# Kernel optimization log

Hardware: AMD Instinct MI355X
Metric: run time of the kernel (lower is better)

The kernel has to match this reference:

```python
import jax, jax.numpy as jnp
import numpy as np

IN_FEATURES = 256
OUT_FEATURES = 128
ALPHA = 0.2  # LeakyReLU negative slope
NEG_INF = -9e15
N_NODES = 8192


def _xavier_uniform(key, shape, gain):
    fan_in, fan_out = shape[0], shape[1]
    limit = gain * np.sqrt(6.0 / (fan_in + fan_out))
    return jax.random.uniform(key, shape, jnp.float32, -limit, limit)


def setup_inputs() -> dict:
    key = jax.random.key(0)
    k_h, k_adj, k_W, k_a = jax.random.split(key, 4)
    h = jax.random.normal(k_h, (N_NODES, IN_FEATURES), dtype=jnp.float32)
    adj = jax.random.randint(k_adj, (N_NODES, N_NODES), 0, 2, dtype=jnp.int32)
    W = _xavier_uniform(k_W, (IN_FEATURES, OUT_FEATURES), gain=1.414)
    a = _xavier_uniform(k_a, (2 * OUT_FEATURES, 1), gain=1.414)
    return {"h": h, "adj": adj, "W": W, "a": a}


def reference(h, adj, W, a):
    # Wh: (N, F_out)
    Wh = h @ W
    # Decompose a = [a1; a2]; e_ij = leakyrelu(Wh_i . a1 + Wh_j . a2)
    # == the original concat([Wh_i, Wh_j]) @ a, without the O(N^2*2F) tensor.
    a1 = a[:OUT_FEATURES, 0]  # (F_out,)
    a2 = a[OUT_FEATURES:, 0]  # (F_out,)
    src = Wh @ a1  # (N,)
    dst = Wh @ a2  # (N,)
    e = jax.nn.leaky_relu(src[:, None] + dst[None, :], negative_slope=ALPHA)  # (N, N)
    attention = jnp.where(adj > 0, e, NEG_INF)
    attention = jax.nn.softmax(attention, axis=1)
    # dropout p=0.0 (eval) -> identity
    h_prime = attention @ Wh  # (N, F_out)
    return jax.nn.elu(h_prime)  # concat=True
```

## Files before the change

kernel.cpp:

```cpp
#include <hip/hip_runtime.h>
#include <hip/hip_bf16.h>

#define N_NODES 8192
#define IN_F    256
#define OUT_F   128
#define ALPHA_S 0.2f

typedef __attribute__((ext_vector_type(8))) short  short8;
typedef __attribute__((ext_vector_type(4))) float  floatx4;
typedef __attribute__((ext_vector_type(4))) int    intx4;
typedef __attribute__((ext_vector_type(4))) float  fx4;

static __device__ __forceinline__ float bf2f(short s) {
    union { unsigned int i; float f; } u;
    u.i = ((unsigned int)(unsigned short)s) << 16;
    return u.f;
}
static __device__ __forceinline__ short f2bf(float f) {
    union { float f; unsigned int i; } u; u.f = f;
    unsigned int r = u.i + 0x7FFFu + ((u.i >> 16) & 1u);
    return (short)(r >> 16);
}

__global__ void k_detect(const unsigned int* __restrict__ hw, int* __restrict__ flag) {
    const int lane = threadIdx.x;
    unsigned int w = hw[lane * 31];
    int e = (w >> 7) & 0xFF;
    unsigned long long b = __ballot(e >= 100 && e <= 140);
    if (lane == 0) *flag = (__popcll(b) >= 40) ? 1 : 0;
}

static __device__ __forceinline__ void load8(const short* p, float* o) {
    short8 v = *(const short8*)p;
#pragma unroll
    for (int j = 0; j < 8; ++j) o[j] = bf2f(v[j]);
}
static __device__ __forceinline__ void load8(const float* p, float* o) {
    float4 v0 = *(const float4*)p;
    float4 v1 = *(const float4*)(p + 4);
    o[0] = v0.x; o[1] = v0.y; o[2] = v0.z; o[3] = v0.w;
    o[4] = v1.x; o[5] = v1.y; o[6] = v1.z; o[7] = v1.w;
}
static __device__ __forceinline__ float to_f(short s)  { return bf2f(s); }
static __device__ __forceinline__ float to_f(float f)  { return f; }

template<typename T>
static __device__ void wh_impl(const T* __restrict__ h, const T* __restrict__ W,
                               const T* __restrict__ a,
                               short* __restrict__ WhT, float* __restrict__ src,
                               float* __restrict__ dst,
                               float* h_tile, short* wh_t, int t, int r_base)
{
    {
        const T* g = h + (size_t)r_base * IN_F;
        float tmp[8];
        load8(g + t * 16, tmp);
#pragma unroll
        for (int j = 0; j < 8; ++j) h_tile[t * 16 + j] = tmp[j];
        load8(g + t * 16 + 8, tmp);
#pragma unroll
        for (int j = 0; j < 8; ++j) h_tile[t * 16 + 8 + j] = tmp[j];
    }
    __syncthreads();

    const int r0   = t >> 4;
    const int fgrp = t & 15;
    const int f0   = fgrp * 8;

    float acc[8];
#pragma unroll
    for (int j = 0; j < 8; ++j) acc[j] = 0.f;

#pragma unroll 4
    for (int k = 0; k < IN_F; ++k) {
        float hf = h_tile[r0 * IN_F + k];
        float wv[8];
        load8(W + (size_t)k * OUT_F + f0, wv);
#pragma unroll
        for (int j = 0; j < 8; ++j)
            acc[j] = fmaf(hf, wv[j], acc[j]);
    }

    float sp = 0.f, dp = 0.f;
#pragma unroll
    for (int j = 0; j < 8; ++j) {
        sp = fmaf(acc[j], to_f(a[f0 + j]), sp);
        dp = fmaf(acc[j], to_f(a[OUT_F + f0 + j]), dp);
    }
#pragma unroll
    for (int m = 1; m < 16; m <<= 1) {
        sp += __shfl_xor(sp, m, 64);
        dp += __shfl_xor(dp, m, 64);
    }
    if (fgrp == 0) {
        src[r_base + r0] = sp;
        dst[r_base + r0] = dp;
    }

#pragma unroll
    for (int j = 0; j < 8; ++j)
        wh_t[(f0 + j) * 32 + r0] = f2bf(acc[j]);
    __syncthreads();
    {
        const int f    = t >> 2;
        const int half = t & 3;
        *(short8*)(WhT + (size_t)f * N_NODES + r_base + half * 8) =
            *(const short8*)&wh_t[f * 32 + half * 8];
    }
}

__global__ __launch_bounds__(512) void k_wh(
    const void* __restrict__ h, const void* __restrict__ W, const void* __restrict__ a,
    const int* __restrict__ flag,
    short* __restrict__ WhT, float* __restrict__ src, float* __restrict__ dst)
{
    __shared__ float h_tile[32 * IN_F];
    __shared__ short wh_t[OUT_F * 32];
    const int t = threadIdx.x;
    const int r_base = blockIdx.x * 32;
    if (*flag)
        wh_impl<short>((const short*)h, (const short*)W, (const short*)a,
                       WhT, src, dst, h_tile, wh_t, t, r_base);
    else
        wh_impl<float>((const float*)h, (const float*)W, (const float*)a,
                       WhT, src, dst, h_tile, wh_t, t, r_base);
}

#define BM 32
#define BK 128
#define WPAD (BK + 8)
#define NIT (N_NODES / BK)

__global__ __launch_bounds__(512) void k_attn(
    const int*   __restrict__ adj,
    const short* __restrict__ WhT,
    const float* __restrict__ src,
    const float* __restrict__ dstv,
    float* __restrict__ out)
{
    __shared__ short wbuf[2][BM * WPAD];
    __shared__ float denom_s[BM];

    const int t    = threadIdx.x;
    const int lane = t & 63;
    const int wave = t >> 6;
    const int r0   = blockIdx.x * BM;

    const int sm  = t >> 4;
    const int sk0 = (t & 15) * 8;
    const float srow = src[r0 + sm];
    const size_t adj_base = (size_t)(r0 + sm) * N_NODES;

    const int ln15 = lane & 15;
    const int q    = lane >> 4;
    const int f0   = wave * 16;
    const short* bbase = WhT + (size_t)(f0 + ln15) * N_NODES + q * 8;

    floatx4 acc0 = {0.f, 0.f, 0.f, 0.f};
    floatx4 acc1 = {0.f, 0.f, 0.f, 0.f};
    floatx4 dac0 = {0.f, 0.f, 0.f, 0.f};
    floatx4 dac1 = {0.f, 0.f, 0.f, 0.f};
    short8 ones;
#pragma unroll
    for (int j = 0; j < 8; ++j) ones[j] = (short)0x3F80;

    auto stage = [&](int it, int buf) {
        const size_t j0 = (size_t)it * BK;
        intx4 m0 = *(const intx4*)(adj + adj_base + j0 + sk0);
        intx4 m1 = *(const intx4*)(adj + adj_base + j0 + sk0 + 4);
        fx4  d0  = *(const fx4*)(dstv + j0 + sk0);
        fx4  d1  = *(const fx4*)(dstv + j0 + sk0 + 4);
        short8 wv;
#pragma unroll
        for (int e = 0; e < 4; ++e) {
            float x = srow + d0[e];
            float l = fmaxf(x, ALPHA_S * x);
            wv[e] = (m0[e] > 0) ? f2bf(__expf(l)) : (short)0;
        }
#pragma unroll
        for (int e = 0; e < 4; ++e) {
            float x = srow + d1[e];
            float l = fmaxf(x, ALPHA_S * x);
            wv[4 + e] = (m1[e] > 0) ? f2bf(__expf(l)) : (short)0;
        }
        *(short8*)&wbuf[buf][sm * WPAD + sk0] = wv;
    };

    auto compute = [&](int it, int buf) {
        const int j0 = it * BK;
        const short* ab = &wbuf[buf][ln15 * WPAD + q * 8];
        const short* bb = bbase + j0;
#pragma unroll
        for (int ks = 0; ks < 4; ++ks) {
            short8 afr0 = *(const short8*)(ab + ks * 32);
            short8 afr1 = *(const short8*)(ab + 16 * WPAD + ks * 32);
            short8 bfr  = *(const short8*)(bb + ks * 32);
            acc0 = __builtin_amdgcn_mfma_f32_16x16x32_bf16(afr0, bfr, acc0, 0, 0, 0);
            acc1 = __builtin_amdgcn_mfma_f32_16x16x32_bf16(afr1, bfr, acc1, 0, 0, 0);
            if (wave == 0) {
                dac0 = __builtin_amdgcn_mfma_f32_16x16x32_bf16(afr0, ones, dac0, 0, 0, 0);
                dac1 = __builtin_amdgcn_mfma_f32_16x16x32_bf16(afr1, ones, dac1, 0, 0, 0);
            }
        }
    };

    stage(0, 0);
    for (int it = 0; it < NIT; ++it) {
        const int p = it & 1;
        __syncthreads();
        if (it + 1 < NIT) stage(it + 1, p ^ 1);
        compute(it, p);
    }

    if (wave == 0 && ln15 == 0) {
#pragma unroll
        for (int r = 0; r < 4; ++r) {
            denom_s[q * 4 + r]      = dac0[r];
            denom_s[16 + q * 4 + r] = dac1[r];
        }
    }
    __syncthreads();
#pragma unroll
    for (int r = 0; r < 4; ++r) {
        const int row0 = q * 4 + r;
        float v0 = acc0[r] / denom_s[row0];
        v0 = v0 > 0.f ? v0 : (__expf(v0) - 1.f);
        out[(size_t)(r0 + row0) * OUT_F + f0 + ln15] = v0;

        const int row1 = 16 + q * 4 + r;
        float v1 = acc1[r] / denom_s[row1];
        v1 = v1 > 0.f ? v1 : (__expf(v1) - 1.f);
        out[(size_t)(r0 + row1) * OUT_F + f0 + ln15] = v1;
    }
}

extern "C" void kernel_launch(void* const* d_in, const int* in_sizes, int n_in,
                              void* d_out, int out_size, void* d_ws, size_t ws_size,
                              hipStream_t stream) {
    const void* h   = d_in[0];
    const int*  adj = (const int*)d_in[1];
    const void* W   = d_in[2];
    const void* a   = d_in[3];
    float* out = (float*)d_out;

    char* ws    = (char*)d_ws;
    int*   flag = (int*)ws;
    short* WhT  = (short*)(ws + 256);
    float* src  = (float*)(ws + 256 + (size_t)OUT_F * N_NODES * 2);
    float* dst  = src + N_NODES;

    k_detect<<<1, 64, 0, stream>>>((const unsigned int*)h, flag);
    k_wh<<<256, 512, 0, stream>>>(h, W, a, flag, WhT, src, dst);
    k_attn<<<256, 512, 0, stream>>>(adj, WhT, src, dst, out);
}
```

Baseline: 475.1 us.

## Split attention over column chunks with atomics, use MFMA for Wh projection

The attention kernel now splits each 32-row group across four column chunks, giving 1024 blocks instead of 256. Partial numerators and denominators are accumulated into the output and a workspace buffer with atomicAdd. A zeroing kernel runs first and a finalize kernel does the normalisation and ELU at the end. The Wh kernel drops the bf16/fp32 runtime detection, computes h@W with bf16 MFMA in shared memory, and computes src/dst via precomputed W·a vectors. The goal is better occupancy and memory-level parallelism over the 256MB adjacency read, at the cost of atomics, two extra launches, and bf16 rounding in the Wh projection.

```diff
diff --git a/kernel.cpp b/kernel.cpp
--- a/kernel.cpp
+++ b/kernel.cpp
@@ -1,5 +1,4 @@
 #include <hip/hip_runtime.h>
-#include <hip/hip_bf16.h>
 
 #define N_NODES 8192
 #define IN_F    256
@@ -7,154 +6,181 @@
 #define ALPHA_S 0.2f
 
 typedef __attribute__((ext_vector_type(8))) short  short8;
+typedef __attribute__((ext_vector_type(4))) short  short4v;
 typedef __attribute__((ext_vector_type(4))) float  floatx4;
 typedef __attribute__((ext_vector_type(4))) int    intx4;
 typedef __attribute__((ext_vector_type(4))) float  fx4;
 
-static __device__ __forceinline__ float bf2f(short s) {
-    union { unsigned int i; float f; } u;
-    u.i = ((unsigned int)(unsigned short)s) << 16;
-    return u.f;
-}
 static __device__ __forceinline__ short f2bf(float f) {
     union { float f; unsigned int i; } u; u.f = f;
     unsigned int r = u.i + 0x7FFFu + ((u.i >> 16) & 1u);
     return (short)(r >> 16);
 }
 
-__global__ void k_detect(const unsigned int* __restrict__ hw, int* __restrict__ flag) {
-    const int lane = threadIdx.x;
-    unsigned int w = hw[lane * 31];
-    int e = (w >> 7) & 0xFF;
-    unsigned long long b = __ballot(e >= 100 && e <= 140);
-    if (lane == 0) *flag = (__popcll(b) >= 40) ? 1 : 0;
-}
-
-static __device__ __forceinline__ void load8(const short* p, float* o) {
-    short8 v = *(const short8*)p;
-#pragma unroll
-    for (int j = 0; j < 8; ++j) o[j] = bf2f(v[j]);
-}
-static __device__ __forceinline__ void load8(const float* p, float* o) {
-    float4 v0 = *(const float4*)p;
-    float4 v1 = *(const float4*)(p + 4);
-    o[0] = v0.x; o[1] = v0.y; o[2] = v0.z; o[3] = v0.w;
-    o[4] = v1.x; o[5] = v1.y; o[6] = v1.z; o[7] = v1.w;
-}
-static __device__ __forceinline__ float to_f(short s)  { return bf2f(s); }
-static __device__ __forceinline__ float to_f(float f)  { return f; }
-
-template<typename T>
-static __device__ void wh_impl(const T* __restrict__ h, const T* __restrict__ W,
-                               const T* __restrict__ a,
-                               short* __restrict__ WhT, float* __restrict__ src,
-                               float* __restrict__ dst,
-                               float* h_tile, short* wh_t, int t, int r_base)
+__global__ void k_zero(float4* __restrict__ out4, float4* __restrict__ den4) {
+    const int i = blockIdx.x * 256 + threadIdx.x;
+    float4 z; z.x = 0.f; z.y = 0.f; z.z = 0.f; z.w = 0.f;
+    if (i < 262144) out4[i] = z;
+    else if (i < 264192) den4[i - 262144] = z;
+}
+
+__global__ __launch_bounds__(512) void k_wh(
+    const float* __restrict__ h,
+    const float* __restrict__ W,
+    const float* __restrict__ a,
+    short* __restrict__ WhT,
+    float* __restrict__ src,
+    float* __restrict__ dst)
 {
-    {
-        const T* g = h + (size_t)r_base * IN_F;
-        float tmp[8];
-        load8(g + t * 16, tmp);
-#pragma unroll
-        for (int j = 0; j < 8; ++j) h_tile[t * 16 + j] = tmp[j];
-        load8(g + t * 16 + 8, tmp);
-#pragma unroll
-        for (int j = 0; j < 8; ++j) h_tile[t * 16 + 8 + j] = tmp[j];
-    }
-    __syncthreads();
+    __shared__ short Wt[OUT_F][IN_F + 8];
+    __shared__ short htile[32][IN_F + 8];
+    __shared__ float q1s[IN_F], q2s[IN_F];
+    __shared__ short wh_t[OUT_F][40];
+
+    const int t      = threadIdx.x;
+    const int lane   = t & 63;
+    const int wave   = t >> 6;
+    const int r_base = blockIdx.x * 32;
+
+#pragma unroll
+    for (int rep = 0; rep < 4; ++rep) {
+        const int idx = rep * 8192 + t * 16;
+        const int k   = idx >> 7;
+        const int f   = idx & 127;
+        fx4 w0 = *(const fx4*)(W + idx);
+        fx4 w1 = *(const fx4*)(W + idx + 4);
+        fx4 w2 = *(const fx4*)(W + idx + 8);
+        fx4 w3 = *(const fx4*)(W + idx + 12);
+        fx4 a10 = *(const fx4*)(a + f);
+        fx4 a11 = *(const fx4*)(a + f + 4);
+        fx4 a12 = *(const fx4*)(a + f + 8);
+        fx4 a13 = *(const fx4*)(a + f + 12);
+        fx4 a20 = *(const fx4*)(a + OUT_F + f);
+        fx4 a21 = *(const fx4*)(a + OUT_F + f + 4);
+        fx4 a22 = *(const fx4*)(a + OUT_F + f + 8);
+        fx4 a23 = *(const fx4*)(a + OUT_F + f + 12);
+        float p1 = 0.f, p2 = 0.f;
+#pragma unroll
+        for (int e = 0; e < 4; ++e) {
+            p1 = fmaf(w0[e], a10[e], p1); p2 = fmaf(w0[e], a20[e], p2);
+            p1 = fmaf(w1[e], a11[e], p1); p2 = fmaf(w1[e], a21[e], p2);
+            p1 = fmaf(w2[e], a12[e], p1); p2 = fmaf(w2[e], a22[e], p2);
+            p1 = fmaf(w3[e], a13[e], p1); p2 = fmaf(w3[e], a23[e], p2);
+        }
+#pragma unroll
+        for (int e = 0; e < 4; ++e) {
+            Wt[f + e][k]      = f2bf(w0[e]);
+            Wt[f + 4 + e][k]  = f2bf(w1[e]);
+            Wt[f + 8 + e][k]  = f2bf(w2[e]);
+            Wt[f + 12 + e][k] = f2bf(w3[e]);
+        }
+#pragma unroll
+        for (int m = 1; m < 8; m <<= 1) {
+            p1 += __shfl_xor(p1, m, 64);
+            p2 += __shfl_xor(p2, m, 64);
+        }
+        if ((t & 7) == 0) { q1s[k] = p1; q2s[k] = p2; }
+    }
 
     const int r0   = t >> 4;
     const int fgrp = t & 15;
-    const int f0   = fgrp * 8;
-
-    float acc[8];
-#pragma unroll
-    for (int j = 0; j < 8; ++j) acc[j] = 0.f;
-
-#pragma unroll 4
-    for (int k = 0; k < IN_F; ++k) {
-        float hf = h_tile[r0 * IN_F + k];
-        float wv[8];
-        load8(W + (size_t)k * OUT_F + f0, wv);
-#pragma unroll
-        for (int j = 0; j < 8; ++j)
-            acc[j] = fmaf(hf, wv[j], acc[j]);
-    }
-
-    float sp = 0.f, dp = 0.f;
-#pragma unroll
-    for (int j = 0; j < 8; ++j) {
-        sp = fmaf(acc[j], to_f(a[f0 + j]), sp);
-        dp = fmaf(acc[j], to_f(a[OUT_F + f0 + j]), dp);
-    }
-#pragma unroll
-    for (int m = 1; m < 16; m <<= 1) {
-        sp += __shfl_xor(sp, m, 64);
-        dp += __shfl_xor(dp, m, 64);
-    }
-    if (fgrp == 0) {
-        src[r_base + r0] = sp;
-        dst[r_base + r0] = dp;
-    }
-
-#pragma unroll
-    for (int j = 0; j < 8; ++j)
-        wh_t[(f0 + j) * 32 + r0] = f2bf(acc[j]);
+    const int k0   = fgrp * 16;
+    fx4 h0, h1, h2, h3;
+    {
+        const float* hp = h + (size_t)(r_base + r0) * IN_F + k0;
+        h0 = *(const fx4*)hp; h1 = *(const fx4*)(hp + 4);
+        h2 = *(const fx4*)(hp + 8); h3 = *(const fx4*)(hp + 12);
+        short8 b0, b1;
+#pragma unroll
+        for (int e = 0; e < 4; ++e) {
+            b0[e]     = f2bf(h0[e]); b0[4 + e] = f2bf(h1[e]);
+            b1[e]     = f2bf(h2[e]); b1[4 + e] = f2bf(h3[e]);
+        }
+        *(short8*)&htile[r0][k0]     = b0;
+        *(short8*)&htile[r0][k0 + 8] = b1;
+    }
+    __syncthreads();
+
+    {
+        float sp = 0.f, dp = 0.f;
+#pragma unroll
+        for (int e = 0; e < 4; ++e) {
+            sp = fmaf(h0[e], q1s[k0 + e], sp);      dp = fmaf(h0[e], q2s[k0 + e], dp);
+            sp = fmaf(h1[e], q1s[k0 + 4 + e], sp);  dp = fmaf(h1[e], q2s[k0 + 4 + e], dp);
+            sp = fmaf(h2[e], q1s[k0 + 8 + e], sp);  dp = fmaf(h2[e], q2s[k0 + 8 + e], dp);
+            sp = fmaf(h3[e], q1s[k0 + 12 + e], sp); dp = fmaf(h3[e], q2s[k0 + 12 + e], dp);
+        }
+#pragma unroll
+        for (int m = 1; m < 16; m <<= 1) {
+            sp += __shfl_xor(sp, m, 64);
+            dp += __shfl_xor(dp, m, 64);
+        }
+        if (fgrp == 0) { src[r_base + r0] = sp; dst[r_base + r0] = dp; }
+    }
+
+    const int ln15 = lane & 15;
+    const int q    = lane >> 4;
+    const int f0   = wave * 16;
+    floatx4 c0 = {0.f, 0.f, 0.f, 0.f};
+    floatx4 c1 = {0.f, 0.f, 0.f, 0.f};
+#pragma unroll
+    for (int s = 0; s < 8; ++s) {
+        short8 bf  = *(const short8*)&Wt[f0 + ln15][s * 32 + q * 8];
+        short8 a0f = *(const short8*)&htile[ln15][s * 32 + q * 8];
+        short8 a1f = *(const short8*)&htile[16 + ln15][s * 32 + q * 8];
+        c0 = __builtin_amdgcn_mfma_f32_16x16x32_bf16(a0f, bf, c0, 0, 0, 0);
+        c1 = __builtin_amdgcn_mfma_f32_16x16x32_bf16(a1f, bf, c1, 0, 0, 0);
+    }
+    {
+        short4v p0, p1;
+#pragma unroll
+        for (int r = 0; r < 4; ++r) { p0[r] = f2bf(c0[r]); p1[r] = f2bf(c1[r]); }
+        *(short4v*)&wh_t[f0 + ln15][q * 4]      = p0;
+        *(short4v*)&wh_t[f0 + ln15][16 + q * 4] = p1;
+    }
     __syncthreads();
     {
         const int f    = t >> 2;
         const int half = t & 3;
         *(short8*)(WhT + (size_t)f * N_NODES + r_base + half * 8) =
-            *(const short8*)&wh_t[f * 32 + half * 8];
-    }
-}
-
-__global__ __launch_bounds__(512) void k_wh(
-    const void* __restrict__ h, const void* __restrict__ W, const void* __restrict__ a,
-    const int* __restrict__ flag,
-    short* __restrict__ WhT, float* __restrict__ src, float* __restrict__ dst)
-{
-    __shared__ float h_tile[32 * IN_F];
-    __shared__ short wh_t[OUT_F * 32];
-    const int t = threadIdx.x;
-    const int r_base = blockIdx.x * 32;
-    if (*flag)
-        wh_impl<short>((const short*)h, (const short*)W, (const short*)a,
-                       WhT, src, dst, h_tile, wh_t, t, r_base);
-    else
-        wh_impl<float>((const float*)h, (const float*)W, (const float*)a,
-                       WhT, src, dst, h_tile, wh_t, t, r_base);
+            *(const short8*)&wh_t[f][half * 8];
+    }
 }
 
 #define BM 32
 #define BK 128
 #define WPAD (BK + 8)
-#define NIT (N_NODES / BK)
-
-__global__ __launch_bounds__(512) void k_attn(
+#define JCH 2048
+#define NIT2 (JCH / BK)
+
+__global__ __launch_bounds__(512, 4) void k_attn(
     const int*   __restrict__ adj,
     const short* __restrict__ WhT,
     const float* __restrict__ src,
     const float* __restrict__ dstv,
-    float* __restrict__ out)
+    float* __restrict__ numer,
+    float* __restrict__ denom)
 {
     __shared__ short wbuf[2][BM * WPAD];
-    __shared__ float denom_s[BM];
 
     const int t    = threadIdx.x;
     const int lane = t & 63;
     const int wave = t >> 6;
-    const int r0   = blockIdx.x * BM;
+    const int rg   = blockIdx.x >> 2;
+    const int jc   = blockIdx.x & 3;
+    const int r0   = rg * BM;
+    const int jb   = jc * JCH;
 
     const int sm  = t >> 4;
     const int sk0 = (t & 15) * 8;
     const float srow = src[r0 + sm];
-    const size_t adj_base = (size_t)(r0 + sm) * N_NODES;
+    const int*   abase = adj  + (size_t)(r0 + sm) * N_NODES + jb + sk0;
+    const float* dbase = dstv + jb + sk0;
 
     const int ln15 = lane & 15;
     const int q    = lane >> 4;
     const int f0   = wave * 16;
-    const short* bbase = WhT + (size_t)(f0 + ln15) * N_NODES + q * 8;
+    const short* bbase = WhT + (size_t)(f0 + ln15) * N_NODES + jb + q * 8;
 
     floatx4 acc0 = {0.f, 0.f, 0.f, 0.f};
     floatx4 acc1 = {0.f, 0.f, 0.f, 0.f};
@@ -164,12 +190,13 @@
 #pragma unroll
     for (int j = 0; j < 8; ++j) ones[j] = (short)0x3F80;
 
-    auto stage = [&](int it, int buf) {
-        const size_t j0 = (size_t)it * BK;
-        intx4 m0 = *(const intx4*)(adj + adj_base + j0 + sk0);
-        intx4 m1 = *(const intx4*)(adj + adj_base + j0 + sk0 + 4);
-        fx4  d0  = *(const fx4*)(dstv + j0 + sk0);
-        fx4  d1  = *(const fx4*)(dstv + j0 + sk0 + 4);
+    intx4 m0 = *(const intx4*)abase;
+    intx4 m1 = *(const intx4*)(abase + 4);
+    fx4   d0 = *(const fx4*)dbase;
+    fx4   d1 = *(const fx4*)(dbase + 4);
+
+    for (int it = 0; it < NIT2; ++it) {
+        const int p = it & 1;
         short8 wv;
 #pragma unroll
         for (int e = 0; e < 4; ++e) {
@@ -183,13 +210,17 @@
             float l = fmaxf(x, ALPHA_S * x);
             wv[4 + e] = (m1[e] > 0) ? f2bf(__expf(l)) : (short)0;
         }
-        *(short8*)&wbuf[buf][sm * WPAD + sk0] = wv;
-    };
-
-    auto compute = [&](int it, int buf) {
-        const int j0 = it * BK;
-        const short* ab = &wbuf[buf][ln15 * WPAD + q * 8];
-        const short* bb = bbase + j0;
+        *(short8*)&wbuf[p][sm * WPAD + sk0] = wv;
+        if (it + 1 < NIT2) {
+            const int o = (it + 1) * BK;
+            m0 = *(const intx4*)(abase + o);
+            m1 = *(const intx4*)(abase + o + 4);
+            d0 = *(const fx4*)(dbase + o);
+            d1 = *(const fx4*)(dbase + o + 4);
+        }
+        __syncthreads();
+        const short* ab = &wbuf[p][ln15 * WPAD + q * 8];
+        const short* bb = bbase + it * BK;
 #pragma unroll
         for (int ks = 0; ks < 4; ++ks) {
             short8 afr0 = *(const short8*)(ab + ks * 32);
@@ -202,54 +233,46 @@
                 dac1 = __builtin_amdgcn_mfma_f32_16x16x32_bf16(afr1, ones, dac1, 0, 0, 0);
             }
         }
-    };
-
-    stage(0, 0);
-    for (int it = 0; it < NIT; ++it) {
-        const int p = it & 1;
-        __syncthreads();
-        if (it + 1 < NIT) stage(it + 1, p ^ 1);
-        compute(it, p);
-    }
-
+    }
+
+#pragma unroll
+    for (int r = 0; r < 4; ++r) {
+        atomicAdd(&numer[(size_t)(r0 + q * 4 + r) * OUT_F + f0 + ln15], acc0[r]);
+        atomicAdd(&numer[(size_t)(r0 + 16 + q * 4 + r) * OUT_F + f0 + ln15], acc1[r]);
+    }
     if (wave == 0 && ln15 == 0) {
 #pragma unroll
         for (int r = 0; r < 4; ++r) {
-            denom_s[q * 4 + r]      = dac0[r];
-            denom_s[16 + q * 4 + r] = dac1[r];
-        }
-    }
-    __syncthreads();
-#pragma unroll
-    for (int r = 0; r < 4; ++r) {
-        const int row0 = q * 4 + r;
-        float v0 = acc0[r] / denom_s[row0];
-        v0 = v0 > 0.f ? v0 : (__expf(v0) - 1.f);
-        out[(size_t)(r0 + row0) * OUT_F + f0 + ln15] = v0;
-
-        const int row1 = 16 + q * 4 + r;
-        float v1 = acc1[r] / denom_s[row1];
-        v1 = v1 > 0.f ? v1 : (__expf(v1) - 1.f);
-        out[(size_t)(r0 + row1) * OUT_F + f0 + ln15] = v1;
-    }
+            atomicAdd(&denom[r0 + q * 4 + r], dac0[r]);
+            atomicAdd(&denom[r0 + 16 + q * 4 + r], dac1[r]);
+        }
+    }
+}
+
+__global__ void k_final(float* __restrict__ out, const float* __restrict__ denom) {
+    const int idx = blockIdx.x * 256 + threadIdx.x;
+    float v = out[idx] / denom[idx >> 7];
+    v = v > 0.f ? v : (__expf(v) - 1.f);
+    out[idx] = v;
 }
 
 extern "C" void kernel_launch(void* const* d_in, const int* in_sizes, int n_in,
                               void* d_out, int out_size, void* d_ws, size_t ws_size,
                               hipStream_t stream) {
-    const void* h   = d_in[0];
-    const int*  adj = (const int*)d_in[1];
-    const void* W   = d_in[2];
-    const void* a   = d_in[3];
+    const float* h   = (const float*)d_in[0];
+    const int*   adj = (const int*)d_in[1];
+    const float* W   = (const float*)d_in[2];
+    const float* a   = (const float*)d_in[3];
     float* out = (float*)d_out;
 
-    char* ws    = (char*)d_ws;
-    int*   flag = (int*)ws;
-    short* WhT  = (short*)(ws + 256);
-    float* src  = (float*)(ws + 256 + (size_t)OUT_F * N_NODES * 2);
-    float* dst  = src + N_NODES;
-
-    k_detect<<<1, 64, 0, stream>>>((const unsigned int*)h, flag);
-    k_wh<<<256, 512, 0, stream>>>(h, W, a, flag, WhT, src, dst);
-    k_attn<<<256, 512, 0, stream>>>(adj, WhT, src, dst, out);
-}
+    char*  ws    = (char*)d_ws;
+    float* denom = (float*)ws;
+    short* WhT   = (short*)(ws + 32768);
+    float* src   = (float*)(ws + 32768 + (size_t)OUT_F * N_NODES * 2);
+    float* dst   = src + N_NODES;
+
+    k_zero <<<1032, 256, 0, stream>>>((float4*)out, (float4*)denom);
+    k_wh   <<<256, 512, 0, stream>>>(h, W, a, WhT, src, dst);
+    k_attn <<<1024, 512, 0, stream>>>(adj, WhT, src, dst, out, denom);
+    k_final<<<4096, 256, 0, stream>>>(out, denom);
+}
```

Measured after the change: 406.8 us. -14.4%, faster.
